# Kernel tuning notes

Hardware: AMD Instinct MI355X
Metric: run time of the kernel (lower is better)

Reference implementation:

```python
import jax, jax.numpy as jnp
import numpy as np

SCALE_DIM = 64  # output_size, used as 1/sqrt(d) scale per source code


def setup_inputs() -> dict:
    key = jax.random.key(0)
    ks = jax.random.split(key, 6)
    B, S, D_IN, D_OUT = 4, 4096, 512, 64
    return {
        "key_inputs": jax.random.normal(ks[0], (B, S, D_IN), dtype=jnp.float32),
        "value_inputs": jax.random.normal(ks[1], (B, S, D_IN), dtype=jnp.float32),
        "query_inputs": jax.random.normal(ks[2], (B, S, D_IN), dtype=jnp.float32),
        "Wq": jax.random.normal(ks[3], (D_IN, D_OUT), dtype=jnp.float32) * 0.05,
        "Wk": jax.random.normal(ks[4], (D_IN, D_OUT), dtype=jnp.float32) * 0.05,
        "Wv": jax.random.normal(ks[5], (D_IN, D_OUT), dtype=jnp.float32) * 0.05,
    }


def reference(key_inputs, value_inputs, query_inputs, Wq, Wk, Wv):
    # QKV projections: [B,S,D_in] x [D_in,D_out] -> [B,S,D_out]
    Q = jnp.einsum("bsd,de->bse", query_inputs, Wq)
    K = jnp.einsum("bsd,de->bse", key_inputs, Wk)
    V = jnp.einsum("bsd,de->bse", value_inputs, Wv)
    d = K.shape[2]
    # scores: [B, Sq, Sk]
    scores = jnp.einsum("bqe,bke->bqk", Q, K) / jnp.sqrt(jnp.float32(d))
    # causal mask: strictly-upper-triangular -inf (source: transpose(tril(-inf, -1)))
    Sq, Sk = Q.shape[1], K.shape[1]
    causal = jnp.tril(jnp.ones((Sq, Sk), dtype=bool))
    scores = jnp.where(causal[None, :, :], scores, -jnp.inf)
    attn = jax.nn.softmax(scores, axis=-1)
    Z = jnp.einsum("bqk,bke->bqe", attn, V)
    return Z
```

## Files before the change

kernel.cpp:

```cpp
#include <hip/hip_runtime.h>
#include <hip/hip_bf16.h>

#define BATCH 4
#define SEQ   4096
#define DIN   512
#define DOUT  64

typedef __attribute__((ext_vector_type(4))) float f32x4;
typedef __attribute__((ext_vector_type(8))) short bf16x8;
typedef __attribute__((ext_vector_type(4))) short bf16x4;

__device__ __forceinline__ f32x4 mfma16(bf16x8 a, bf16x8 b, f32x4 c) {
    return __builtin_amdgcn_mfma_f32_16x16x32_bf16(a, b, c, 0, 0, 0);
}
__device__ __forceinline__ f32x4 mfma16k(bf16x4 a, bf16x4 b, f32x4 c) {
    return __builtin_amdgcn_mfma_f32_16x16x16bf16_1k(a, b, c, 0, 0, 0);
}

__device__ __forceinline__ short f2bf(float f) {
    union { float f; unsigned u; } x; x.f = f;
    unsigned r = x.u + 0x7FFFu + ((x.u >> 16) & 1u);
    return (short)(r >> 16);
}

__device__ __forceinline__ unsigned pack_bf2(float lo, float hi) {
    union { float f; unsigned u; } a, b; a.f = lo; b.f = hi;
    return __builtin_amdgcn_perm(b.u, a.u, 0x07060302u);
}

__device__ __forceinline__ void dma16(const void* g, void* l) {
    __builtin_amdgcn_global_load_lds(
        (const __attribute__((address_space(1))) void*)g,
        (__attribute__((address_space(3))) void*)l, 16, 0, 0);
}

#define QSCALE 0.1803368801111204f

__global__ __launch_bounds__(256) void wconv_kernel(
    const float* __restrict__ Wq, const float* __restrict__ Wk,
    const float* __restrict__ Wv, short* __restrict__ Wt)
{
    const int m = blockIdx.y;
    const float* W = (m == 0) ? Wq : (m == 1) ? Wk : Wv;
    const int idx = blockIdx.x * 256 + threadIdx.x;
    const int k = idx >> 6;
    const int n = idx & 63;
    Wt[m * (DOUT * DIN) + n * DIN + k] = f2bf(W[idx]);
}

__global__ __launch_bounds__(256, 4) void proj_kernel(
    const float* __restrict__ Xq, const float* __restrict__ Xk, const float* __restrict__ Xv,
    const short* __restrict__ Wt,
    short* __restrict__ Qb, short* __restrict__ Kb, short* __restrict__ Vt)
{
    const int m = blockIdx.y;
    const float* X  = (m == 0) ? Xq : (m == 1) ? Xk : Xv;
    const short* Wm = Wt + m * (DOUT * DIN);

    const int tid  = threadIdx.x;
    const int wv   = tid >> 6;
    const int lane = tid & 63;
    const int quad = lane >> 4;
    const int l16  = lane & 15;
    const long waveRow = (long)blockIdx.x * 64 + wv * 16;

    const float* xg = X  + (waveRow + l16) * DIN + quad * 8;
    const short* wg = Wm + (long)l16 * DIN + quad * 8;

    f32x4 acc[4];
    #pragma unroll
    for (int e = 0; e < 4; ++e) acc[e] = (f32x4){0.f, 0.f, 0.f, 0.f};

    #pragma unroll 2
    for (int kt = 0; kt < 8; ++kt) {
        const float* xk = xg + kt * 64;
        const short* wk = wg + kt * 64;
        #pragma unroll
        for (int c2 = 0; c2 < 2; ++c2) {
            float4 xa = *(const float4*)(xk + c2 * 32);
            float4 xc = *(const float4*)(xk + c2 * 32 + 4);
            bf16x8 af;
            af[0] = f2bf(xa.x); af[1] = f2bf(xa.y); af[2] = f2bf(xa.z); af[3] = f2bf(xa.w);
            af[4] = f2bf(xc.x); af[5] = f2bf(xc.y); af[6] = f2bf(xc.z); af[7] = f2bf(xc.w);
            #pragma unroll
            for (int e = 0; e < 4; ++e) {
                bf16x8 bf = *(const bf16x8*)(wk + (long)e * 16 * DIN + c2 * 32);
                if (m < 2) acc[e] = mfma16(af, bf, acc[e]);
                else       acc[e] = mfma16(bf, af, acc[e]);
            }
        }
    }

    if (m < 2) {
        short* O = (m == 0) ? Qb : Kb;
        const float sc = (m == 0) ? QSCALE : 1.0f;
        #pragma unroll
        for (int e = 0; e < 4; ++e)
            #pragma unroll
            for (int r = 0; r < 4; ++r)
                O[(waveRow + quad * 4 + r) * DOUT + e * 16 + l16] = f2bf(acc[e][r] * sc);
    } else {
        const long b = waveRow >> 12;
        const long s = waveRow & (SEQ - 1);
        #pragma unroll
        for (int e = 0; e < 4; ++e)
            #pragma unroll
            for (int r = 0; r < 4; ++r)
                Vt[(b * DOUT + e * 16 + quad * 4 + r) * SEQ + s + l16] = f2bf(acc[e][r]);
    }
}

__global__ __launch_bounds__(512, 4) void flash_kernel(
    const short* __restrict__ Qb, const short* __restrict__ Kb,
    const short* __restrict__ Vt, float* __restrict__ Out)
{
    __shared__ __align__(16) char smem[2][32768];

    const int i    = blockIdx.x;
    const int b    = (i & 7) >> 1;
    const int half = i >> 8;
    const int v    = (((i >> 3) & 31) << 1) | (i & 1);
    const int t    = half ? v : (127 - v);

    const int tid  = threadIdx.x;
    const int wv   = tid >> 6;
    const int lane = tid & 63;
    const int quad = lane >> 4;
    const int l16  = lane & 15;
    const int wq   = wv >> 2;
    const int wk   = wv & 3;
    const int q0w  = t * 32 + wq * 16;

    const short* Qp = Qb + ((long)b * SEQ + q0w + l16) * DOUT + quad * 8;
    bf16x8 qf0 = *(const bf16x8*)(Qp);
    bf16x8 qf1 = *(const bf16x8*)(Qp + 32);

    const short* Kbase  = Kb + (long)b * SEQ * DOUT;
    const short* VbaseG = Vt + (long)b * DOUT * SEQ;

    const short* gk = Kbase + (long)(wv * 16 + l16) * DOUT + quad * 8;
    const int erow = 4 * wv + quad;
    const int cgr  = l16 ^ (erow & 15);
    const short* gv = VbaseG + (long)erow * SEQ + cgr * 8;

    f32x4 acc[4];
    #pragma unroll
    for (int e = 0; e < 4; ++e) acc[e] = (f32x4){0.f, 0.f, 0.f, 0.f};
    float mrow = -1e30f, lrow = 0.f;

    const int q_hi   = q0w + 15;
    const int qg     = q0w + l16;
    const int wfirst = wk * 32;
    const int R      = t / 4 + 1;

#define STAGE_KV(B, KV0) do {                                         \
        char* kb_ = &smem[(B)][0];                                    \
        char* vb_ = &smem[(B)][0] + 16384;                            \
        const short* gkp_ = gk + (long)(KV0) * DOUT;                  \
        dma16(gkp_,      kb_ + (2 * wv) * 1024);                      \
        dma16(gkp_ + 32, kb_ + (2 * wv + 1) * 1024);                  \
        const short* gvp_ = gv + (KV0);                               \
        dma16(gvp_,            vb_ + (wv)     * 1024);                \
        dma16(gvp_ + 32 * SEQ, vb_ + (wv + 8) * 1024);                \
    } while (0)

    STAGE_KV(0, 0);
    __syncthreads();

    for (int r = 0; r < R; ++r) {
        const int kv0 = r * 128;
        const int cur = r & 1;
        if (r + 1 < R) STAGE_KV(cur ^ 1, kv0 + 128);

        if ((kv0 + wfirst) <= q_hi) {
            const char* kb = &smem[cur][0];
            const char* vb = &smem[cur][0] + 16384;

            f32x4 sc[2];
            #pragma unroll
            for (int kh = 0; kh < 2; ++kh) {
                const int slot = (wk * 2 + kh) * 2;
                bf16x8 k0 = *(const bf16x8*)(kb + slot * 1024 + lane * 16);
                bf16x8 k1 = *(const bf16x8*)(kb + (slot + 1) * 1024 + lane * 16);
                f32x4 z = (f32x4){0.f, 0.f, 0.f, 0.f};
                z = mfma16(k0, qf0, z);
                z = mfma16(k1, qf1, z);
                sc[kh] = z;
            }

            if (kv0 + wfirst + 31 > q0w) {
                #pragma unroll
                for (int kh = 0; kh < 2; ++kh)
                    #pragma unroll
                    for (int rr = 0; rr < 4; ++rr)
                        sc[kh][rr] = ((kv0 + wfirst + kh * 16 + quad * 4 + rr) <= qg)
                                   ? sc[kh][rr] : -1e30f;
            }

            float tm = fmaxf(fmaxf(fmaxf(sc[0][0], sc[0][1]), fmaxf(sc[0][2], sc[0][3])),
                             fmaxf(fmaxf(sc[1][0], sc[1][1]), fmaxf(sc[1][2], sc[1][3])));
            tm = fmaxf(tm, __shfl_xor(tm, 16, 64));
            tm = fmaxf(tm, __shfl_xor(tm, 32, 64));
            if (!__all(tm <= mrow)) {
                const float mn = fmaxf(mrow, tm);
                const float alpha = __builtin_amdgcn_exp2f(mrow - mn);
                mrow = mn;
                lrow *= alpha;
                #pragma unroll
                for (int e = 0; e < 4; ++e)
                    #pragma unroll
                    for (int rr = 0; rr < 4; ++rr) acc[e][rr] *= alpha;
            }
            float p[2][4];
            float rs0 = 0.f, rs1 = 0.f;
            #pragma unroll
            for (int kh = 0; kh < 2; ++kh)
                #pragma unroll
                for (int rr = 0; rr < 4; ++rr) {
                    p[kh][rr] = __builtin_amdgcn_exp2f(sc[kh][rr] - mrow);
                    if (kh == 0) rs0 += p[kh][rr]; else rs1 += p[kh][rr];
                }
            float rs = rs0 + rs1;
            rs += __shfl_xor(rs, 16, 64);
            rs += __shfl_xor(rs, 32, 64);
            lrow += rs;

            union { unsigned u[2]; bf16x4 v; } pf[2];
            #pragma unroll
            for (int kh = 0; kh < 2; ++kh) {
                pf[kh].u[0] = pack_bf2(p[kh][0], p[kh][1]);
                pf[kh].u[1] = pack_bf2(p[kh][2], p[kh][3]);
            }

            #pragma unroll
            for (int kh = 0; kh < 2; ++kh) {
                const int gbase = wk * 4 + kh * 2 + (quad >> 1);
                #pragma unroll
                for (int et = 0; et < 4; ++et) {
                    const int e = et * 16 + l16;
                    bf16x4 cv = *(const bf16x4*)(vb + e * 256
                                   + ((gbase ^ (e & 15)) * 16) + (quad & 1) * 8);
                    acc[et] = mfma16k(cv, pf[kh].v, acc[et]);
                }
            }
        }
        __syncthreads();
    }
#undef STAGE_KV

    float* s_m   = (float*)&smem[0][0];
    float* s_l   = s_m + 128;
    float* s_acc = s_l + 128;

    if (quad == 0) { s_m[wv * 16 + l16] = mrow; s_l[wv * 16 + l16] = lrow; }
    #pragma unroll
    for (int et = 0; et < 4; ++et)
        #pragma unroll
        for (int rr = 0; rr < 4; ++rr)
            s_acc[(wv * 16 + l16) * 65 + et * 16 + quad * 4 + rr] = acc[et][rr];
    __syncthreads();

    const int col   = tid & 63;
    const int rbase = (tid >> 6) * 4;
    float* outp = Out + ((long)b * SEQ + t * 32) * DOUT;
    #pragma unroll
    for (int k = 0; k < 4; ++k) {
        const int row = rbase + k;
        const int w0  = (row >> 4) * 4;
        const int lr  = row & 15;
        const float m0 = s_m[(w0 + 0) * 16 + lr];
        const float m1 = s_m[(w0 + 1) * 16 + lr];
        const float m2 = s_m[(w0 + 2) * 16 + lr];
        const float m3 = s_m[(w0 + 3) * 16 + lr];
        const float mM = fmaxf(fmaxf(m0, m1), fmaxf(m2, m3));
        const float a0 = __builtin_amdgcn_exp2f(m0 - mM);
        const float a1 = __builtin_amdgcn_exp2f(m1 - mM);
        const float a2 = __builtin_amdgcn_exp2f(m2 - mM);
        const float a3 = __builtin_amdgcn_exp2f(m3 - mM);
        const float li = a0 * s_l[(w0 + 0) * 16 + lr] + a1 * s_l[(w0 + 1) * 16 + lr]
                       + a2 * s_l[(w0 + 2) * 16 + lr] + a3 * s_l[(w0 + 3) * 16 + lr];
        const float o  = a0 * s_acc[((w0 + 0) * 16 + lr) * 65 + col]
                       + a1 * s_acc[((w0 + 1) * 16 + lr) * 65 + col]
                       + a2 * s_acc[((w0 + 2) * 16 + lr) * 65 + col]
                       + a3 * s_acc[((w0 + 3) * 16 + lr) * 65 + col];
        outp[row * DOUT + col] = o / li;
    }
}

extern "C" void kernel_launch(void* const* d_in, const int* in_sizes, int n_in,
                              void* d_out, int out_size, void* d_ws, size_t ws_size,
                              hipStream_t stream) {
    const float* key_in   = (const float*)d_in[0];
    const float* value_in = (const float*)d_in[1];
    const float* query_in = (const float*)d_in[2];
    const float* Wq = (const float*)d_in[3];
    const float* Wk = (const float*)d_in[4];
    const float* Wv = (const float*)d_in[5];
    float* out = (float*)d_out;

    short* Qb = (short*)d_ws;
    short* Kb = Qb + (long)BATCH * SEQ * DOUT;
    short* Vt = Kb + (long)BATCH * SEQ * DOUT;
    short* Wt = Vt + (long)BATCH * SEQ * DOUT;

    dim3 wgrid((DOUT * DIN) / 256, 3);
    wconv_kernel<<<wgrid, 256, 0, stream>>>(Wq, Wk, Wv, Wt);

    dim3 pgrid(BATCH * SEQ / 64, 3);
    proj_kernel<<<pgrid, 256, 0, stream>>>(query_in, key_in, value_in,
                                           Wt, Qb, Kb, Vt);

    flash_kernel<<<dim3(SEQ / 32 * BATCH), 512, 0, stream>>>(Qb, Kb, Vt, out);
}
```

Before: 180.6 us.

## Stage projection inputs through double-buffered LDS with async DMA, weights in registers

The projection kernel is restructured so each wave keeps its 16-column slice of the bf16 weight matrix in registers. The 64 fp32 input rows are streamed into two XOR-swizzled LDS buffers with direct global-to-LDS 16-byte loads, 16 rows per round. Each round waits on vmcnt, runs 16 MFMAs and refills the freed buffer while storing results. This removes the repeated per-wave global weight loads and overlaps input loading with compute. In exchange it uses 64KB of LDS per block and drops the occupancy hint from 4 to 2.

```diff
diff --git a/kernel.cpp b/kernel.cpp
--- a/kernel.cpp
+++ b/kernel.cpp
@@ -48,11 +48,13 @@
     Wt[m * (DOUT * DIN) + n * DIN + k] = f2bf(W[idx]);
 }
 
-__global__ __launch_bounds__(256, 4) void proj_kernel(
+__global__ __launch_bounds__(256, 2) void proj_kernel(
     const float* __restrict__ Xq, const float* __restrict__ Xk, const float* __restrict__ Xv,
     const short* __restrict__ Wt,
     short* __restrict__ Qb, short* __restrict__ Kb, short* __restrict__ Vt)
 {
+    __shared__ __align__(16) char smem[2][32768];
+
     const int m = blockIdx.y;
     const float* X  = (m == 0) ? Xq : (m == 1) ? Xk : Xv;
     const short* Wm = Wt + m * (DOUT * DIN);
@@ -62,52 +64,84 @@
     const int lane = tid & 63;
     const int quad = lane >> 4;
     const int l16  = lane & 15;
-    const long waveRow = (long)blockIdx.x * 64 + wv * 16;
-
-    const float* xg = X  + (waveRow + l16) * DIN + quad * 8;
-    const short* wg = Wm + (long)l16 * DIN + quad * 8;
-
-    f32x4 acc[4];
-    #pragma unroll
-    for (int e = 0; e < 4; ++e) acc[e] = (f32x4){0.f, 0.f, 0.f, 0.f};
-
-    #pragma unroll 2
-    for (int kt = 0; kt < 8; ++kt) {
-        const float* xk = xg + kt * 64;
-        const short* wk = wg + kt * 64;
+    const long blockRow = (long)blockIdx.x * 64;
+
+    bf16x8 WB[16];
+    {
+        const short* wp = Wm + (long)(wv * 16 + l16) * DIN + quad * 8;
         #pragma unroll
-        for (int c2 = 0; c2 < 2; ++c2) {
-            float4 xa = *(const float4*)(xk + c2 * 32);
-            float4 xc = *(const float4*)(xk + c2 * 32 + 4);
-            bf16x8 af;
-            af[0] = f2bf(xa.x); af[1] = f2bf(xa.y); af[2] = f2bf(xa.z); af[3] = f2bf(xa.w);
-            af[4] = f2bf(xc.x); af[5] = f2bf(xc.y); af[6] = f2bf(xc.z); af[7] = f2bf(xc.w);
-            #pragma unroll
-            for (int e = 0; e < 4; ++e) {
-                bf16x8 bf = *(const bf16x8*)(wk + (long)e * 16 * DIN + c2 * 32);
-                if (m < 2) acc[e] = mfma16(af, bf, acc[e]);
-                else       acc[e] = mfma16(bf, af, acc[e]);
-            }
-        }
+        for (int c = 0; c < 16; ++c) WB[c] = *(const bf16x8*)(wp + c * 32);
     }
-
-    if (m < 2) {
-        short* O = (m == 0) ? Qb : Kb;
-        const float sc = (m == 0) ? QSCALE : 1.0f;
-        #pragma unroll
-        for (int e = 0; e < 4; ++e)
-            #pragma unroll
-            for (int r = 0; r < 4; ++r)
-                O[(waveRow + quad * 4 + r) * DOUT + e * 16 + l16] = f2bf(acc[e][r] * sc);
-    } else {
-        const long b = waveRow >> 12;
-        const long s = waveRow & (SEQ - 1);
-        #pragma unroll
-        for (int e = 0; e < 4; ++e)
-            #pragma unroll
-            for (int r = 0; r < 4; ++r)
-                Vt[(b * DOUT + e * 16 + quad * 4 + r) * SEQ + s + l16] = f2bf(acc[e][r]);
-    }
+    __builtin_amdgcn_sched_barrier(0);
+
+#define STAGE_X(B, R) do {                                                 \
+        char* xb_ = &smem[(B)][0];                                         \
+        _Pragma("unroll")                                                  \
+        for (int rr_ = 0; rr_ < 4; ++rr_) {                                \
+            const int rl_ = 4 * wv + rr_;                                  \
+            const float* rp_ = X + (blockRow + (R) * 16 + rl_) * DIN;      \
+            _Pragma("unroll")                                              \
+            for (int h_ = 0; h_ < 2; ++h_) {                               \
+                const int g_ = (h_ * 32 + (lane >> 1)) ^ rl_;              \
+                dma16(rp_ + g_ * 8 + (lane & 1) * 4,                       \
+                      xb_ + rl_ * 2048 + h_ * 1024);                       \
+            }                                                              \
+        }                                                                  \
+    } while (0)
+
+    STAGE_X(0, 0);
+    STAGE_X(1, 1);
+    __builtin_amdgcn_sched_barrier(0);
+
+    const float sc = (m == 0) ? QSCALE : 1.0f;
+    short* O = (m == 0) ? Qb : Kb;
+    const long vb = blockRow >> 12;
+
+#define ROUND(R, WAITI, DOSTAGE) do {                                      \
+        __builtin_amdgcn_sched_barrier(0);                                 \
+        asm volatile("s_waitcnt vmcnt(" #WAITI ")" ::: "memory");          \
+        __builtin_amdgcn_sched_barrier(0);                                 \
+        __builtin_amdgcn_s_barrier();            \
+        const char* xb = &smem[(R) & 1][0];                                \
+        f32x4 acc = (f32x4){0.f, 0.f, 0.f, 0.f};                           \
+        _Pragma("unroll")                                                  \
+        for (int c = 0; c < 16; ++c) {                                     \
+            const char* xp = xb + l16 * 2048                               \
+                               + (((c * 4 + quad) ^ l16) * 32);            \
+            float4 xa = *(const float4*)(xp);                              \
+            float4 xc = *(const float4*)(xp + 16);                         \
+            bf16x8 af;                                                     \
+            af[0] = f2bf(xa.x); af[1] = f2bf(xa.y);                        \
+            af[2] = f2bf(xa.z); af[3] = f2bf(xa.w);                        \
+            af[4] = f2bf(xc.x); af[5] = f2bf(xc.y);                        \
+            af[6] = f2bf(xc.z); af[7] = f2bf(xc.w);                        \
+            if (m < 2) acc = mfma16(af, WB[c], acc);                       \
+            else       acc = mfma16(WB[c], af, acc);                       \
+        }                                                                  \
+        if (DOSTAGE) {                                                     \
+            __builtin_amdgcn_s_barrier();         \
+            STAGE_X((R) & 1, (R) + 2);                                     \
+        }                                                                  \
+        if (m < 2) {                                                       \
+            _Pragma("unroll")                                              \
+            for (int rr = 0; rr < 4; ++rr)                                 \
+                O[(blockRow + (R) * 16 + quad * 4 + rr) * DOUT             \
+                  + wv * 16 + l16] = f2bf(acc[rr] * sc);                   \
+        } else {                                                           \
+            const long s0 = (blockRow + (R) * 16) & (SEQ - 1);             \
+            _Pragma("unroll")                                              \
+            for (int rr = 0; rr < 4; ++rr)                                 \
+                Vt[(vb * DOUT + wv * 16 + quad * 4 + rr) * SEQ + s0 + l16] \
+                    = f2bf(acc[rr]);                                       \
+        }                                                                  \
+    } while (0)
+
+    ROUND(0, 8,  1);
+    ROUND(1, 12, 1);
+    ROUND(2, 12, 0);
+    ROUND(3, 0,  0);
+#undef ROUND
+#undef STAGE_X
 }
 
 __global__ __launch_bounds__(512, 4) void flash_kernel(
```

Result: faster. 170.9 us (-5.4%).
